# Performance work log

Measured on AMD Instinct MI355X. Metric: run time of the kernel, lower is better.

## Reference

```python
import jax, jax.numpy as jnp
import numpy as np

N = 20000
E = 320000
F_IN = 256
HID = 32
HEADS = 8
EDGE_DIM = HID // 4  # 8
NEG_SLOPE = 0.2


def _gat_conv(x, src, dst, e_emb, W, att_s, att_d, W_e, att_e, bias, H, C):
    """PyG-style GATConv with edge_dim, add_self_loops=True (fill_value='mean'), concat heads."""
    n = x.shape[0]
    loop = jnp.arange(n, dtype=src.dtype)
    # self-loop edge_attr = scatter-mean of edge_attr by dst (0 for isolated nodes)
    deg = jax.ops.segment_sum(jnp.ones_like(dst, dtype=x.dtype), dst, num_segments=n)
    e_mean = jax.ops.segment_sum(e_emb, dst, num_segments=n) / jnp.maximum(deg, 1.0)[:, None]
    src_a = jnp.concatenate([src, loop])
    dst_a = jnp.concatenate([dst, loop])
    e_all = jnp.concatenate([e_emb, e_mean], axis=0)  # [E+N, edge_dim]

    h = (x @ W).reshape(n, H, C)                      # [N,H,C]
    a_src = jnp.einsum('nhc,hc->nh', h, att_s)        # [N,H]
    a_dst = jnp.einsum('nhc,hc->nh', h, att_d)
    he = (e_all @ W_e).reshape(-1, H, C)              # [E+N,H,C]
    a_edge = jnp.einsum('ehc,hc->eh', he, att_e)      # [E+N,H]

    alpha = jax.nn.leaky_relu(a_src[src_a] + a_dst[dst_a] + a_edge, NEG_SLOPE)
    # segment softmax over destination nodes
    amax = jax.ops.segment_max(alpha, dst_a, num_segments=n)
    alpha = jnp.exp(alpha - amax[dst_a])
    denom = jax.ops.segment_sum(alpha, dst_a, num_segments=n)
    alpha = alpha / (denom[dst_a] + 1e-16)

    msg = h[src_a] * alpha[:, :, None]                # [E+N,H,C]
    out = jax.ops.segment_sum(msg, dst_a, num_segments=n)  # [N,H,C]
    return out.reshape(n, H * C) + bias


def setup_inputs() -> dict:
    key = jax.random.key(0)
    ks = jax.random.split(key, 16)

    def glorot(k, shape):
        fan_in, fan_out = shape[0], shape[-1]
        s = np.sqrt(6.0 / (fan_in + fan_out))
        return jax.random.uniform(k, shape, jnp.float32, -s, s)

    x = jax.random.normal(ks[0], (N, F_IN), jnp.float32)
    edge_index = jax.random.randint(ks[1], (2, E), 0, N, jnp.int32)
    edge_attr = jax.random.uniform(ks[2], (E, 2), jnp.float32)

    # spatial_embed: Linear(2 -> EDGE_DIM)
    Wse = glorot(ks[3], (2, EDGE_DIM))
    bse = jnp.zeros((EDGE_DIM,), jnp.float32)
    # conv1: in=F_IN, heads=HEADS, out=HID, edge_dim=EDGE_DIM
    W1 = glorot(ks[4], (F_IN, HEADS * HID))
    as1 = glorot(ks[5], (HEADS, HID))
    ad1 = glorot(ks[6], (HEADS, HID))
    We1 = glorot(ks[7], (EDGE_DIM, HEADS * HID))
    ae1 = glorot(ks[8], (HEADS, HID))
    b1 = jnp.zeros((HEADS * HID,), jnp.float32)
    # conv2: in=HEADS*HID, heads=1, out=HID
    W2 = glorot(ks[9], (HEADS * HID, HID))
    as2 = glorot(ks[10], (1, HID))
    ad2 = glorot(ks[11], (1, HID))
    We2 = glorot(ks[12], (EDGE_DIM, HID))
    ae2 = glorot(ks[13], (1, HID))
    b2 = jnp.zeros((HID,), jnp.float32)

    return {"x": x, "edge_index": edge_index, "edge_attr": edge_attr,
            "Wse": Wse, "bse": bse,
            "W1": W1, "as1": as1, "ad1": ad1, "We1": We1, "ae1": ae1, "b1": b1,
            "W2": W2, "as2": as2, "ad2": ad2, "We2": We2, "ae2": ae2, "b2": b2}


def reference(x, edge_index, edge_attr, Wse, bse,
              W1, as1, ad1, We1, ae1, b1,
              W2, as2, ad2, We2, ae2, b2):
    src, dst = edge_index[0], edge_index[1]
    e = jax.nn.relu(edge_attr @ Wse + bse)            # [E, EDGE_DIM]
    h = _gat_conv(x, src, dst, e, W1, as1, ad1, We1, ae1, b1, HEADS, HID)
    h = jax.nn.relu(h)                                # dropout inactive (eval)
    out = _gat_conv(h, src, dst, e, W2, as2, ad2, We2, ae2, b2, 1, HID)
    return out
```

## Files before the change

### kernel.cpp

```cpp
#include <hip/hip_runtime.h>
#include <float.h>


typedef short v8s __attribute__((ext_vector_type(8)));
typedef float v4f __attribute__((ext_vector_type(4)));

__device__ __forceinline__ ushort f2bf(float f) {
  unsigned u = __float_as_uint(f);
  u = (u + 0x7FFF + ((u >> 16) & 1)) >> 16;
  return (ushort)u;
}
__device__ __forceinline__ float bf2f(ushort h) {
  return __uint_as_float(((unsigned)h) << 16);
}

__global__ __launch_bounds__(1024) void k_scan(const int* __restrict__ deg,
                                               int* __restrict__ row_ptr, int N) {
  __shared__ int part[1024];
  int tid = threadIdx.x;
  int chunk = (N + 1023) / 1024;
  int lo = tid * chunk;
  if (lo > N) lo = N;
  int hi = lo + chunk;
  if (hi > N) hi = N;
  int s = 0;
  for (int i = lo; i < hi; i++) s += deg[i];
  part[tid] = s;
  __syncthreads();
  for (int off = 1; off < 1024; off <<= 1) {
    int v = 0;
    if (tid >= off) v = part[tid - off];
    __syncthreads();
    part[tid] += v;
    __syncthreads();
  }
  int base = part[tid] - s;
  for (int i = lo; i < hi; i++) { row_ptr[i] = base; base += deg[i]; }
  if (tid == 1023) row_ptr[N] = part[1023];
}

__global__ void k_scatter(const int* __restrict__ src, const int* __restrict__ dst,
                          const int* __restrict__ row_ptr, int* __restrict__ cursor,
                          const float* __restrict__ aed1_lin, const float* __restrict__ aed2_lin,
                          int* __restrict__ csr_src, float* __restrict__ csr_aed1,
                          float* __restrict__ csr_aed2, int E) {
  int i = blockIdx.x * blockDim.x + threadIdx.x;
  if (i >= E) return;
  int d = dst[i];
  int pos = row_ptr[d] + atomicAdd(&cursor[d], 1);
  csr_src[pos] = src[i];
  const float4* a4 = (const float4*)(aed1_lin + (size_t)i * 8);
  *(float4*)(csr_aed1 + (size_t)pos * 8)     = a4[0];
  *(float4*)(csr_aed1 + (size_t)pos * 8 + 4) = a4[1];
  csr_aed2[pos] = aed2_lin[i];
}

__global__ __launch_bounds__(256) void k_prep_trans(const float* __restrict__ W1,
                                                    const float* __restrict__ We1,
                                                    const float* __restrict__ ae1,
                                                    const float* __restrict__ We2,
                                                    const float* __restrict__ ae2,
                                                    ushort* __restrict__ Bt,
                                                    float* __restrict__ M1,
                                                    float* __restrict__ m2) {
  if (blockIdx.x == 64) {
    int t = threadIdx.x;
    if (t < 64) {
      int k = t >> 3, h = t & 7;
      float s = 0.f;
      for (int c = 0; c < 32; c++) s += We1[k * 256 + h * 32 + c] * ae1[h * 32 + c];
      M1[k * 8 + h] = s;
    } else if (t < 72) {
      int k = t - 64;
      float s = 0.f;
      for (int c = 0; c < 32; c++) s += We2[k * 32 + c] * ae2[c];
      m2[k] = s;
    }
    return;
  }
  __shared__ float tile[32][33];
  int bx = blockIdx.x & 7, by = blockIdx.x >> 3;
  int tx = threadIdx.x & 31, ty = threadIdx.x >> 5;
  for (int r = ty; r < 32; r += 8)
    tile[r][tx] = W1[(size_t)(by * 32 + r) * 256 + bx * 32 + tx];
  __syncthreads();
  for (int r = ty; r < 32; r += 8)
    Bt[(size_t)(bx * 32 + r) * 256 + by * 32 + tx] = f2bf(tile[tx][r]);
}

__global__ void k_edge_fused(const float* __restrict__ ea, const int* __restrict__ dst,
                             const float* __restrict__ Wse, const float* __restrict__ bse,
                             const float* __restrict__ M1, const float* __restrict__ m2,
                             float* __restrict__ aed1, float* __restrict__ aed2,
                             int* __restrict__ deg, int E) {
  __shared__ float sW[16], sb[8], sM[64], sm2[8];
  int t = threadIdx.x;
  if (t < 16) sW[t] = Wse[t];
  if (t < 8) sb[t] = bse[t];
  if (t < 64) sM[t] = M1[t];
  if (t >= 64 && t < 72) sm2[t - 64] = m2[t - 64];
  __syncthreads();
  int e = blockIdx.x * blockDim.x + t;
  if (e >= E) return;
  atomicAdd(&deg[dst[e]], 1);
  float2 av = ((const float2*)ea)[e];
  float e8[8];
#pragma unroll
  for (int k = 0; k < 8; k++)
    e8[k] = fmaxf(av.x * sW[k] + av.y * sW[8 + k] + sb[k], 0.f);
  float o[8];
#pragma unroll
  for (int h = 0; h < 8; h++) {
    float s = 0.f;
#pragma unroll
    for (int k = 0; k < 8; k++) s += e8[k] * sM[k * 8 + h];
    o[h] = s;
  }
  *(float4*)(aed1 + (size_t)e * 8)     = make_float4(o[0], o[1], o[2], o[3]);
  *(float4*)(aed1 + (size_t)e * 8 + 4) = make_float4(o[4], o[5], o[6], o[7]);
  float s2 = 0.f;
#pragma unroll
  for (int k = 0; k < 8; k++) s2 += e8[k] * sm2[k];
  aed2[e] = s2;
}

__global__ __launch_bounds__(256) void k_gemm1_mfma(const float* __restrict__ A,
                                                    const ushort* __restrict__ Bt,
                                                    const float* __restrict__ as1,
                                                    const float* __restrict__ ad1,
                                                    ushort* __restrict__ h1b,
                                                    float* __restrict__ asv,
                                                    float* __restrict__ adv, int M) {
  __shared__ ushort sA[64 * 40];
  __shared__ ushort sB[256 * 40];
  __shared__ float sas[256], sad[256];
  int t = threadIdx.x;
  int wave = t >> 6, lane = t & 63;
  int m0 = blockIdx.x * 64;
  int c = lane & 15, kg = lane >> 4;
  sas[t] = as1[t];
  sad[t] = ad1[t];
  v4f acc[4][4];
#pragma unroll
  for (int a = 0; a < 4; a++)
#pragma unroll
    for (int b = 0; b < 4; b++) acc[a][b] = (v4f)(0.f);
  int arow = t >> 2;
  int akoff = (t & 3) * 8;
  bool aval = (m0 + arow) < M;
  const float* aptr = A + (size_t)(m0 + arow) * 256 + akoff;
  const ushort* bptr = Bt + (size_t)t * 256;
  for (int k0 = 0; k0 < 256; k0 += 32) {
    float4 v0 = make_float4(0.f, 0.f, 0.f, 0.f), v1 = v0;
    if (aval) { v0 = *(const float4*)(aptr + k0); v1 = *(const float4*)(aptr + k0 + 4); }
    ushort* dst = &sA[arow * 40 + akoff];
    dst[0] = f2bf(v0.x); dst[1] = f2bf(v0.y); dst[2] = f2bf(v0.z); dst[3] = f2bf(v0.w);
    dst[4] = f2bf(v1.x); dst[5] = f2bf(v1.y); dst[6] = f2bf(v1.z); dst[7] = f2bf(v1.w);
    *(v8s*)&sB[t * 40 + 0]  = *(const v8s*)(bptr + k0 + 0);
    *(v8s*)&sB[t * 40 + 8]  = *(const v8s*)(bptr + k0 + 8);
    *(v8s*)&sB[t * 40 + 16] = *(const v8s*)(bptr + k0 + 16);
    *(v8s*)&sB[t * 40 + 24] = *(const v8s*)(bptr + k0 + 24);
    __syncthreads();
    v8s af[4], bfr[4];
#pragma unroll
    for (int mt = 0; mt < 4; mt++) af[mt] = *(v8s*)&sA[(mt * 16 + c) * 40 + kg * 8];
#pragma unroll
    for (int nt = 0; nt < 4; nt++) bfr[nt] = *(v8s*)&sB[(wave * 64 + nt * 16 + c) * 40 + kg * 8];
#pragma unroll
    for (int mt = 0; mt < 4; mt++)
#pragma unroll
      for (int nt = 0; nt < 4; nt++)
        acc[mt][nt] = __builtin_amdgcn_mfma_f32_16x16x32_bf16(af[mt], bfr[nt], acc[mt][nt], 0, 0, 0);
    __syncthreads();
  }
  int colbase = wave * 64;
#pragma unroll
  for (int mt = 0; mt < 4; mt++) {
#pragma unroll
    for (int i = 0; i < 4; i++) {
      int m = m0 + mt * 16 + kg * 4 + i;
      if (m < M) {
#pragma unroll
        for (int nt = 0; nt < 4; nt++)
          h1b[(size_t)m * 256 + colbase + nt * 16 + c] = f2bf(acc[mt][nt][i]);
      }
      float s1a = acc[mt][0][i] * sas[colbase + c]      + acc[mt][1][i] * sas[colbase + 16 + c];
      float s2a = acc[mt][0][i] * sad[colbase + c]      + acc[mt][1][i] * sad[colbase + 16 + c];
      float s1b = acc[mt][2][i] * sas[colbase + 32 + c] + acc[mt][3][i] * sas[colbase + 48 + c];
      float s2b = acc[mt][2][i] * sad[colbase + 32 + c] + acc[mt][3][i] * sad[colbase + 48 + c];
#pragma unroll
      for (int o = 1; o < 16; o <<= 1) {
        s1a += __shfl_xor(s1a, o);
        s2a += __shfl_xor(s2a, o);
        s1b += __shfl_xor(s1b, o);
        s2b += __shfl_xor(s2b, o);
      }
      if (c == 0 && m < M) {
        asv[(size_t)m * 8 + 2 * wave]     = s1a;
        adv[(size_t)m * 8 + 2 * wave]     = s2a;
        asv[(size_t)m * 8 + 2 * wave + 1] = s1b;
        adv[(size_t)m * 8 + 2 * wave + 1] = s2b;
      }
    }
  }
}

__global__ __launch_bounds__(64) void k_conv1(
    const int* __restrict__ row_ptr, const int* __restrict__ csr_src,
    const float* __restrict__ csr_aed1, const float* __restrict__ asv,
    const float* __restrict__ adv, const ushort* __restrict__ h1b,
    const float* __restrict__ b1, ushort* __restrict__ h2b, int N) {
  int n = blockIdx.x;
  int lane = threadIdx.x;
  int h = lane >> 3;
  int sub = lane & 7;
  int hh = lane & 7;
  __shared__ float sw[64 * 8];
  __shared__ int ssrc[64];
  __shared__ float sm[8], sl[8], sadv[8], smean[8];
  int begin = row_ptr[n], end = row_ptr[n + 1];
  int degr = end - begin;
  if (lane < 8) { sm[lane] = -FLT_MAX; sl[lane] = 0.f; sadv[lane] = adv[(size_t)n * 8 + lane]; }
  float aedsum = 0.f;
  float4 acc = make_float4(0.f, 0.f, 0.f, 0.f);
  for (int cs = begin; cs < end; cs += 64) {
    int c = min(64, end - cs);
    __syncthreads();
    if (lane < c) ssrc[lane] = csr_src[cs + lane];
    __syncthreads();
    for (int idx = lane; idx < c * 8; idx += 64) {
      int el = idx >> 3;
      float ae = csr_aed1[(size_t)(cs + el) * 8 + hh];
      aedsum += ae;
      float a = asv[(size_t)ssrc[el] * 8 + hh] + sadv[hh] + ae;
      a = a > 0.f ? a : 0.2f * a;
      sw[idx] = a;
    }
    __syncthreads();
    float mloc = -FLT_MAX;
    for (int el = sub; el < c; el += 8) mloc = fmaxf(mloc, sw[el * 8 + h]);
#pragma unroll
    for (int o = 1; o < 8; o <<= 1) mloc = fmaxf(mloc, __shfl_xor(mloc, o));
    float mold = sm[h];
    float mnew = fmaxf(mold, mloc);
    float scale = __expf(mold - mnew);
    float lloc = 0.f;
    for (int el = sub; el < c; el += 8) {
      float w = __expf(sw[el * 8 + h] - mnew);
      sw[el * 8 + h] = w;
      lloc += w;
    }
#pragma unroll
    for (int o = 1; o < 8; o <<= 1) lloc += __shfl_xor(lloc, o);
    __syncthreads();
    if (sub == 0) { sm[h] = mnew; sl[h] = sl[h] * scale + lloc; }
    acc.x *= scale; acc.y *= scale; acc.z *= scale; acc.w *= scale;
    for (int el = 0; el < c; el++) {
      float w = sw[el * 8 + h];
      ushort4 hv = *(const ushort4*)(h1b + (size_t)ssrc[el] * 256 + lane * 4);
      acc.x += w * bf2f(hv.x);
      acc.y += w * bf2f(hv.y);
      acc.z += w * bf2f(hv.z);
      acc.w += w * bf2f(hv.w);
    }
  }
  aedsum += __shfl_xor(aedsum, 8);
  aedsum += __shfl_xor(aedsum, 16);
  aedsum += __shfl_xor(aedsum, 32);
  float invd = 1.f / (float)(degr > 1 ? degr : 1);
  if (lane < 8) smean[lane] = aedsum * invd;
  __syncthreads();
  float a_self = asv[(size_t)n * 8 + h] + sadv[h] + smean[h];
  a_self = a_self > 0.f ? a_self : 0.2f * a_self;
  float mold = sm[h];
  float mnew = fmaxf(mold, a_self);
  float scale = __expf(mold - mnew);
  float w_self = __expf(a_self - mnew);
  float l_fin = sl[h] * scale + w_self;
  ushort4 hs = *(const ushort4*)(h1b + (size_t)n * 256 + lane * 4);
  acc.x = acc.x * scale + w_self * bf2f(hs.x);
  acc.y = acc.y * scale + w_self * bf2f(hs.y);
  acc.z = acc.z * scale + w_self * bf2f(hs.z);
  acc.w = acc.w * scale + w_self * bf2f(hs.w);
  float inv = 1.f / (l_fin + 1e-16f);
  float4 bv = *(const float4*)(b1 + lane * 4);
  ushort4 o4;
  o4.x = f2bf(fmaxf(acc.x * inv + bv.x, 0.f));
  o4.y = f2bf(fmaxf(acc.y * inv + bv.y, 0.f));
  o4.z = f2bf(fmaxf(acc.z * inv + bv.z, 0.f));
  o4.w = f2bf(fmaxf(acc.w * inv + bv.w, 0.f));
  *(ushort4*)(h2b + (size_t)n * 256 + lane * 4) = o4;
}

__global__ __launch_bounds__(256) void k_gemm2(const ushort* __restrict__ h2b,
                                               const float* __restrict__ W2,
                                               const float* __restrict__ as2,
                                               const float* __restrict__ ad2,
                                               float* __restrict__ g2,
                                               float* __restrict__ asv2,
                                               float* __restrict__ adv2, int N) {
  __shared__ float xs[8 * 256];
  __shared__ float sas[32], sad[32];
  int t = threadIdx.x;
  if (t < 32) { sas[t] = as2[t]; sad[t] = ad2[t]; }
  int n0 = blockIdx.x * 8;
  for (int idx = t; idx < 8 * 256; idx += 256) {
    int node = n0 + (idx >> 8);
    xs[idx] = (node < N) ? bf2f(h2b[(size_t)node * 256 + (idx & 255)]) : 0.f;
  }
  __syncthreads();
  int j = t >> 5, cc = t & 31;
  int node = n0 + j;
  float acc = 0.f;
#pragma unroll 8
  for (int k = 0; k < 256; k++) acc += xs[j * 256 + k] * W2[k * 32 + cc];
  float s1 = acc * sas[cc], s2 = acc * sad[cc];
#pragma unroll
  for (int o = 1; o < 32; o <<= 1) {
    s1 += __shfl_xor(s1, o);
    s2 += __shfl_xor(s2, o);
  }
  if (node < N) {
    g2[(size_t)node * 32 + cc] = acc;
    if (cc == 0) { asv2[node] = s1; adv2[node] = s2; }
  }
}

__global__ __launch_bounds__(64) void k_conv2(
    const int* __restrict__ row_ptr, const int* __restrict__ csr_src,
    const float* __restrict__ csr_aed2, const float* __restrict__ asv2,
    const float* __restrict__ adv2, const float* __restrict__ g2,
    const float* __restrict__ b2, float* __restrict__ out, int N) {
  int n = blockIdx.x;
  int lane = threadIdx.x;
  int sub = lane >> 3, q = lane & 7;
  __shared__ float sw[64];
  __shared__ int ssrc[64];
  int begin = row_ptr[n], end = row_ptr[n + 1];
  int degr = end - begin;
  float advn = adv2[n];
  float m = -FLT_MAX, l = 0.f, aedsum = 0.f;
  float4 acc = make_float4(0.f, 0.f, 0.f, 0.f);
  for (int cs = begin; cs < end; cs += 64) {
    int c = min(64, end - cs);
    __syncthreads();
    float a = -FLT_MAX;
    if (lane < c) {
      int s = csr_src[cs + lane];
      ssrc[lane] = s;
      float ae = csr_aed2[cs + lane];
      aedsum += ae;
      a = asv2[s] + advn + ae;
      a = a > 0.f ? a : 0.2f * a;
    }
    float cm = a;
#pragma unroll
    for (int o = 1; o < 64; o <<= 1) cm = fmaxf(cm, __shfl_xor(cm, o));
    float nm = fmaxf(m, cm);
    float sc = __expf(m - nm);
    float w = (lane < c) ? __expf(a - nm) : 0.f;
    float cl = w;
#pragma unroll
    for (int o = 1; o < 64; o <<= 1) cl += __shfl_xor(cl, o);
    l = l * sc + cl;
    m = nm;
    sw[lane] = w;
    __syncthreads();
    acc.x *= sc; acc.y *= sc; acc.z *= sc; acc.w *= sc;
    for (int el = sub; el < c; el += 8) {
      float w2 = sw[el];
      const float4 gv = *(const float4*)(g2 + (size_t)ssrc[el] * 32 + q * 4);
      acc.x += w2 * gv.x; acc.y += w2 * gv.y; acc.z += w2 * gv.z; acc.w += w2 * gv.w;
    }
  }
#pragma unroll
  for (int o = 1; o < 64; o <<= 1) aedsum += __shfl_xor(aedsum, o);
  float invd = 1.f / (float)(degr > 1 ? degr : 1);
  float a_self = asv2[n] + advn + aedsum * invd;
  a_self = a_self > 0.f ? a_self : 0.2f * a_self;
  float nm = fmaxf(m, a_self);
  float sc = __expf(m - nm);
  float w_self = __expf(a_self - nm);
  l = l * sc + w_self;
  acc.x *= sc; acc.y *= sc; acc.z *= sc; acc.w *= sc;
  if (sub == 0) {
    const float4 gv = *(const float4*)(g2 + (size_t)n * 32 + q * 4);
    acc.x += w_self * gv.x; acc.y += w_self * gv.y;
    acc.z += w_self * gv.z; acc.w += w_self * gv.w;
  }
#pragma unroll
  for (int o = 8; o < 64; o <<= 1) {
    acc.x += __shfl_xor(acc.x, o);
    acc.y += __shfl_xor(acc.y, o);
    acc.z += __shfl_xor(acc.z, o);
    acc.w += __shfl_xor(acc.w, o);
  }
  if (lane < 8) {
    float inv = 1.f / (l + 1e-16f);
    float4 bv = *(const float4*)(b2 + lane * 4);
    float4 o4;
    o4.x = acc.x * inv + bv.x;
    o4.y = acc.y * inv + bv.y;
    o4.z = acc.z * inv + bv.z;
    o4.w = acc.w * inv + bv.w;
    *(float4*)(out + (size_t)n * 32 + lane * 4) = o4;
  }
}

extern "C" void kernel_launch(void* const* d_in, const int* in_sizes, int n_in,
                              void* d_out, int out_size, void* d_ws, size_t ws_size,
                              hipStream_t stream) {
  (void)n_in; (void)out_size; (void)ws_size;
  const float* x   = (const float*)d_in[0];
  const int*   ei  = (const int*)d_in[1];
  const float* ea  = (const float*)d_in[2];
  const float* Wse = (const float*)d_in[3];
  const float* bse = (const float*)d_in[4];
  const float* W1  = (const float*)d_in[5];
  const float* as1 = (const float*)d_in[6];
  const float* ad1 = (const float*)d_in[7];
  const float* We1 = (const float*)d_in[8];
  const float* ae1 = (const float*)d_in[9];
  const float* b1  = (const float*)d_in[10];
  const float* W2  = (const float*)d_in[11];
  const float* as2 = (const float*)d_in[12];
  const float* ad2 = (const float*)d_in[13];
  const float* We2 = (const float*)d_in[14];
  const float* ae2 = (const float*)d_in[15];
  const float* b2  = (const float*)d_in[16];
  const int N = in_sizes[0] / 256;
  const int E = in_sizes[1] / 2;
  const int* src = ei;
  const int* dst = ei + E;

  char* base = (char*)d_ws;
  size_t off = 0;
  auto alloc = [&](size_t bytes) -> char* {
    off = (off + 255) & ~(size_t)255;
    char* p = base + off;
    off += bytes;
    return p;
  };
  int*   deg      = (int*)alloc((size_t)N * 4);
  int*   cursor   = (int*)alloc((size_t)N * 4);
  size_t zero_bytes = (size_t)((char*)(cursor + N) - (char*)deg);
  int* row_ptr    = (int*)alloc((size_t)(N + 1) * 4);
  int* csr_src    = (int*)alloc((size_t)E * 4);
  float* aed1_lin = (float*)alloc((size_t)E * 8 * 4);
  float* aed2_lin = (float*)alloc((size_t)E * 4);
  float* csr_aed1 = (float*)alloc((size_t)E * 8 * 4);
  float* csr_aed2 = (float*)alloc((size_t)E * 4);
  ushort* W1T     = (ushort*)alloc((size_t)256 * 256 * 2);
  ushort* h1b     = (ushort*)alloc((size_t)N * 256 * 2);
  float* asv1     = (float*)alloc((size_t)N * 8 * 4);
  float* adv1     = (float*)alloc((size_t)N * 8 * 4);
  ushort* h2b     = (ushort*)alloc((size_t)N * 256 * 2);
  float* g2       = (float*)alloc((size_t)N * 32 * 4);
  float* asv2     = (float*)alloc((size_t)N * 4);
  float* adv2     = (float*)alloc((size_t)N * 4);
  float* M1       = (float*)alloc(64 * 4);
  float* m2       = (float*)alloc(8 * 4);

  hipMemsetAsync(deg, 0, zero_bytes, stream);
  k_prep_trans<<<65, 256, 0, stream>>>(W1, We1, ae1, We2, ae2, W1T, M1, m2);
  k_edge_fused<<<(E + 255) / 256, 256, 0, stream>>>(ea, dst, Wse, bse, M1, m2,
                                                    aed1_lin, aed2_lin, deg, E);
  k_scan<<<1, 1024, 0, stream>>>(deg, row_ptr, N);
  k_scatter<<<(E + 255) / 256, 256, 0, stream>>>(src, dst, row_ptr, cursor,
                                                 aed1_lin, aed2_lin,
                                                 csr_src, csr_aed1, csr_aed2, E);
  k_gemm1_mfma<<<(N + 63) / 64, 256, 0, stream>>>(x, W1T, as1, ad1, h1b, asv1, adv1, N);
  k_conv1<<<N, 64, 0, stream>>>(row_ptr, csr_src, csr_aed1, asv1, adv1, h1b, b1, h2b, N);
  k_gemm2<<<(N + 7) / 8, 256, 0, stream>>>(h2b, W2, as2, ad2, g2, asv2, adv2, N);
  k_conv2<<<N, 64, 0, stream>>>(row_ptr, csr_src, csr_aed2, asv2, adv2, g2, b2,
                                (float*)d_out, N);
}
```

Before: 258.3 us.

## Fuse edge attention precompute into CSR scatter and merge degree count with prep

The degree-count atomics and the W1 transpose / M1 precompute now run as one kernel launch, using block ranges to pick the work. The edge embedding and attention projection move into the scatter kernel, which writes straight to CSR positions. This drops the intermediate aed1_lin/aed2_lin buffers and one launch. The GEMM A-tile bf16 conversion also stores packed 32-bit pairs instead of individual 16-bit writes.

Measured after the change: 257.0 us. No clear change (-0.5%).

```diff
diff --git a/kernel.cpp b/kernel.cpp
--- a/kernel.cpp
+++ b/kernel.cpp
@@ -1,4 +1,5 @@
 #include <hip/hip_runtime.h>
+#include <hip/hip_bf16.h>
 #include <float.h>
 
 
@@ -12,6 +13,52 @@
 }
 __device__ __forceinline__ float bf2f(ushort h) {
   return __uint_as_float(((unsigned)h) << 16);
+}
+__device__ __forceinline__ unsigned pk2bf(float lo, float hi) {
+  return (unsigned)f2bf(lo) | ((unsigned)f2bf(hi) << 16);
+}
+
+__global__ __launch_bounds__(256) void k_pre(const int* __restrict__ dst,
+                                             const float* __restrict__ W1,
+                                             const float* __restrict__ We1,
+                                             const float* __restrict__ ae1,
+                                             const float* __restrict__ We2,
+                                             const float* __restrict__ ae2,
+                                             int* __restrict__ deg,
+                                             ushort* __restrict__ Bt,
+                                             float* __restrict__ M1,
+                                             float* __restrict__ m2,
+                                             int E, int DB) {
+  int b = blockIdx.x;
+  if (b < DB) {
+    int e = b * 256 + threadIdx.x;
+    if (e < E) atomicAdd(&deg[dst[e]], 1);
+    return;
+  }
+  if (b == DB + 64) {
+    int t = threadIdx.x;
+    if (t < 64) {
+      int k = t >> 3, h = t & 7;
+      float s = 0.f;
+      for (int c = 0; c < 32; c++) s += We1[k * 256 + h * 32 + c] * ae1[h * 32 + c];
+      M1[k * 8 + h] = s;
+    } else if (t < 72) {
+      int k = t - 64;
+      float s = 0.f;
+      for (int c = 0; c < 32; c++) s += We2[k * 32 + c] * ae2[c];
+      m2[k] = s;
+    }
+    return;
+  }
+  int b2 = b - DB;
+  __shared__ float tile[32][33];
+  int bx = b2 & 7, by = b2 >> 3;
+  int tx = threadIdx.x & 31, ty = threadIdx.x >> 5;
+  for (int r = ty; r < 32; r += 8)
+    tile[r][tx] = W1[(size_t)(by * 32 + r) * 256 + bx * 32 + tx];
+  __syncthreads();
+  for (int r = ty; r < 32; r += 8)
+    Bt[(size_t)(bx * 32 + r) * 256 + by * 32 + tx] = f2bf(tile[tx][r]);
 }
 
 __global__ __launch_bounds__(1024) void k_scan(const int* __restrict__ deg,
@@ -40,59 +87,12 @@
 }
 
 __global__ void k_scatter(const int* __restrict__ src, const int* __restrict__ dst,
+                          const float* __restrict__ ea,
+                          const float* __restrict__ Wse, const float* __restrict__ bse,
+                          const float* __restrict__ M1, const float* __restrict__ m2,
                           const int* __restrict__ row_ptr, int* __restrict__ cursor,
-                          const float* __restrict__ aed1_lin, const float* __restrict__ aed2_lin,
                           int* __restrict__ csr_src, float* __restrict__ csr_aed1,
                           float* __restrict__ csr_aed2, int E) {
-  int i = blockIdx.x * blockDim.x + threadIdx.x;
-  if (i >= E) return;
-  int d = dst[i];
-  int pos = row_ptr[d] + atomicAdd(&cursor[d], 1);
-  csr_src[pos] = src[i];
-  const float4* a4 = (const float4*)(aed1_lin + (size_t)i * 8);
-  *(float4*)(csr_aed1 + (size_t)pos * 8)     = a4[0];
-  *(float4*)(csr_aed1 + (size_t)pos * 8 + 4) = a4[1];
-  csr_aed2[pos] = aed2_lin[i];
-}
-
-__global__ __launch_bounds__(256) void k_prep_trans(const float* __restrict__ W1,
-                                                    const float* __restrict__ We1,
-                                                    const float* __restrict__ ae1,
-                                                    const float* __restrict__ We2,
-                                                    const float* __restrict__ ae2,
-                                                    ushort* __restrict__ Bt,
-                                                    float* __restrict__ M1,
-                                                    float* __restrict__ m2) {
-  if (blockIdx.x == 64) {
-    int t = threadIdx.x;
-    if (t < 64) {
-      int k = t >> 3, h = t & 7;
-      float s = 0.f;
-      for (int c = 0; c < 32; c++) s += We1[k * 256 + h * 32 + c] * ae1[h * 32 + c];
-      M1[k * 8 + h] = s;
-    } else if (t < 72) {
-      int k = t - 64;
-      float s = 0.f;
-      for (int c = 0; c < 32; c++) s += We2[k * 32 + c] * ae2[c];
-      m2[k] = s;
-    }
-    return;
-  }
-  __shared__ float tile[32][33];
-  int bx = blockIdx.x & 7, by = blockIdx.x >> 3;
-  int tx = threadIdx.x & 31, ty = threadIdx.x >> 5;
-  for (int r = ty; r < 32; r += 8)
-    tile[r][tx] = W1[(size_t)(by * 32 + r) * 256 + bx * 32 + tx];
-  __syncthreads();
-  for (int r = ty; r < 32; r += 8)
-    Bt[(size_t)(bx * 32 + r) * 256 + by * 32 + tx] = f2bf(tile[tx][r]);
-}
-
-__global__ void k_edge_fused(const float* __restrict__ ea, const int* __restrict__ dst,
-                             const float* __restrict__ Wse, const float* __restrict__ bse,
-                             const float* __restrict__ M1, const float* __restrict__ m2,
-                             float* __restrict__ aed1, float* __restrict__ aed2,
-                             int* __restrict__ deg, int E) {
   __shared__ float sW[16], sb[8], sM[64], sm2[8];
   int t = threadIdx.x;
   if (t < 16) sW[t] = Wse[t];
@@ -100,10 +100,9 @@
   if (t < 64) sM[t] = M1[t];
   if (t >= 64 && t < 72) sm2[t - 64] = m2[t - 64];
   __syncthreads();
-  int e = blockIdx.x * blockDim.x + t;
-  if (e >= E) return;
-  atomicAdd(&deg[dst[e]], 1);
-  float2 av = ((const float2*)ea)[e];
+  int i = blockIdx.x * blockDim.x + t;
+  if (i >= E) return;
+  float2 av = ((const float2*)ea)[i];
   float e8[8];
 #pragma unroll
   for (int k = 0; k < 8; k++)
@@ -116,12 +115,15 @@
     for (int k = 0; k < 8; k++) s += e8[k] * sM[k * 8 + h];
     o[h] = s;
   }
-  *(float4*)(aed1 + (size_t)e * 8)     = make_float4(o[0], o[1], o[2], o[3]);
-  *(float4*)(aed1 + (size_t)e * 8 + 4) = make_float4(o[4], o[5], o[6], o[7]);
   float s2 = 0.f;
 #pragma unroll
   for (int k = 0; k < 8; k++) s2 += e8[k] * sm2[k];
-  aed2[e] = s2;
+  int d = dst[i];
+  int pos = row_ptr[d] + atomicAdd(&cursor[d], 1);
+  csr_src[pos] = src[i];
+  *(float4*)(csr_aed1 + (size_t)pos * 8)     = make_float4(o[0], o[1], o[2], o[3]);
+  *(float4*)(csr_aed1 + (size_t)pos * 8 + 4) = make_float4(o[4], o[5], o[6], o[7]);
+  csr_aed2[pos] = s2;
 }
 
 __global__ __launch_bounds__(256) void k_gemm1_mfma(const float* __restrict__ A,
@@ -153,9 +155,11 @@
   for (int k0 = 0; k0 < 256; k0 += 32) {
     float4 v0 = make_float4(0.f, 0.f, 0.f, 0.f), v1 = v0;
     if (aval) { v0 = *(const float4*)(aptr + k0); v1 = *(const float4*)(aptr + k0 + 4); }
-    ushort* dst = &sA[arow * 40 + akoff];
-    dst[0] = f2bf(v0.x); dst[1] = f2bf(v0.y); dst[2] = f2bf(v0.z); dst[3] = f2bf(v0.w);
-    dst[4] = f2bf(v1.x); dst[5] = f2bf(v1.y); dst[6] = f2bf(v1.z); dst[7] = f2bf(v1.w);
+    unsigned* dst32 = (unsigned*)&sA[arow * 40 + akoff];
+    dst32[0] = pk2bf(v0.x, v0.y);
+    dst32[1] = pk2bf(v0.z, v0.w);
+    dst32[2] = pk2bf(v1.x, v1.y);
+    dst32[3] = pk2bf(v1.z, v1.w);
     *(v8s*)&sB[t * 40 + 0]  = *(const v8s*)(bptr + k0 + 0);
     *(v8s*)&sB[t * 40 + 8]  = *(const v8s*)(bptr + k0 + 8);
     *(v8s*)&sB[t * 40 + 16] = *(const v8s*)(bptr + k0 + 16);
@@ -446,8 +450,6 @@
   size_t zero_bytes = (size_t)((char*)(cursor + N) - (char*)deg);
   int* row_ptr    = (int*)alloc((size_t)(N + 1) * 4);
   int* csr_src    = (int*)alloc((size_t)E * 4);
-  float* aed1_lin = (float*)alloc((size_t)E * 8 * 4);
-  float* aed2_lin = (float*)alloc((size_t)E * 4);
   float* csr_aed1 = (float*)alloc((size_t)E * 8 * 4);
   float* csr_aed2 = (float*)alloc((size_t)E * 4);
   ushort* W1T     = (ushort*)alloc((size_t)256 * 256 * 2);
@@ -461,14 +463,12 @@
   float* M1       = (float*)alloc(64 * 4);
   float* m2       = (float*)alloc(8 * 4);
 
+  const int DB = (E + 255) / 256;
   hipMemsetAsync(deg, 0, zero_bytes, stream);
-  k_prep_trans<<<65, 256, 0, stream>>>(W1, We1, ae1, We2, ae2, W1T, M1, m2);
-  k_edge_fused<<<(E + 255) / 256, 256, 0, stream>>>(ea, dst, Wse, bse, M1, m2,
-                                                    aed1_lin, aed2_lin, deg, E);
+  k_pre<<<DB + 65, 256, 0, stream>>>(dst, W1, We1, ae1, We2, ae2, deg, W1T, M1, m2, E, DB);
   k_scan<<<1, 1024, 0, stream>>>(deg, row_ptr, N);
-  k_scatter<<<(E + 255) / 256, 256, 0, stream>>>(src, dst, row_ptr, cursor,
-                                                 aed1_lin, aed2_lin,
-                                                 csr_src, csr_aed1, csr_aed2, E);
+  k_scatter<<<DB, 256, 0, stream>>>(src, dst, ea, Wse, bse, M1, m2, row_ptr, cursor,
+                                    csr_src, csr_aed1, csr_aed2, E);
   k_gemm1_mfma<<<(N + 63) / 64, 256, 0, stream>>>(x, W1T, as1, ad1, h1b, asv1, adv1, N);
   k_conv1<<<N, 64, 0, stream>>>(row_ptr, csr_src, csr_aed1, asv1, adv1, h1b, b1, h2b, N);
   k_gemm2<<<(N + 7) / 8, 256, 0, stream>>>(h2b, W2, as2, ad2, g2, asv2, adv2, N);
```
